# Kernel optimization log

Measured on AMD Instinct MI355X. Metric: run time of the kernel, lower is better.

The kernel has to match this reference:

```python
import jax, jax.numpy as jnp
import numpy as np

DIM = 256
DIM_HEAD = 32
NUM_HEADS = DIM // DIM_HEAD
SCALE = DIM_HEAD ** -0.5


def setup_inputs() -> dict:
    key = jax.random.key(0)
    ks = jax.random.split(key, 5)
    B, L, C = 4, 2048, DIM
    x = jax.random.normal(ks[0], (B, L, C), dtype=jnp.float32)
    # Linear weights stored torch-style: (out_features, in_features)
    w_qkv = jax.random.normal(ks[1], (3 * C, C), dtype=jnp.float32) * (C ** -0.5)
    b_qkv = jax.random.normal(ks[2], (3 * C,), dtype=jnp.float32) * 0.02
    w_proj = jax.random.normal(ks[3], (C, C), dtype=jnp.float32) * (C ** -0.5)
    b_proj = jax.random.normal(ks[4], (C,), dtype=jnp.float32) * 0.02
    return {"x": x, "w_qkv": w_qkv, "b_qkv": b_qkv, "w_proj": w_proj, "b_proj": b_proj}


def reference(x, w_qkv, b_qkv, w_proj, b_proj):
    B, L, C = x.shape
    H, D = NUM_HEADS, DIM_HEAD
    qkv = x @ w_qkv.T + b_qkv                      # (B, L, 3C)
    qkv = qkv.reshape(B, L, H, 3 * D).transpose(0, 2, 1, 3)  # (B, H, L, 3D)
    q, k, v = jnp.split(qkv, 3, axis=-1)           # each (B, H, L, D)
    attn = jnp.einsum('bhld,bhmd->bhlm', q, k) * SCALE
    attn = jax.nn.softmax(attn, axis=-1)
    out = jnp.einsum('bhlm,bhmd->bhld', attn, v)   # (B, H, L, D)
    out = out.transpose(0, 2, 1, 3).reshape(B, L, C)
    return out @ w_proj.T + b_proj
```

## Files before the change

### kernel.cpp

```cpp
#include <hip/hip_runtime.h>
#include <hip/hip_bf16.h>


typedef __bf16 bf16x4 __attribute__((ext_vector_type(4)));
typedef __bf16 bf16x8 __attribute__((ext_vector_type(8)));
typedef float  f32x4  __attribute__((ext_vector_type(4)));
typedef float  f32x16 __attribute__((ext_vector_type(16)));
typedef unsigned u32x4 __attribute__((ext_vector_type(4)));

#define MFMA16(a, b, c) __builtin_amdgcn_mfma_f32_16x16x32_bf16((a), (b), (c), 0, 0, 0)
#define MFMA32(a, b, c) __builtin_amdgcn_mfma_f32_32x32x16_bf16((a), (b), (c), 0, 0, 0)

static constexpr int Bsz = 4, L = 2048, C = 256, H = 8, D = 32;
static constexpr float SCALE = 0.17677669529663687f;
static constexpr float LOG2E = 1.44269504088896f;
static constexpr float QSCALE = SCALE * LOG2E;

__device__ inline float fast_exp2(float x) {
#if __has_builtin(__builtin_amdgcn_exp2f)
    return __builtin_amdgcn_exp2f(x);
#else
    float r; asm("v_exp_f32 %0, %1" : "=v"(r) : "v"(x)); return r;
#endif
}

__device__ inline unsigned cvt_pk_bf16(float lo, float hi) {
    unsigned d;
    asm("v_cvt_pk_bf16_f32 %0, %1, %2" : "=v"(d) : "v"(lo), "v"(hi));
    return d;
}

__global__ __launch_bounds__(256) void qkv_gemm(
    const float* __restrict__ X, const float* __restrict__ W,
    const float* __restrict__ Bq,
    __bf16* __restrict__ Qw, __bf16* __restrict__ Kw, __bf16* __restrict__ Vt)
{
    constexpr int LDK = 136;
    __shared__ __align__(16) __bf16 smem[128 * LDK + 64 * LDK];
    __bf16* Xs = smem;
    __bf16* Wsh = smem + 128 * LDK;

    const int bm = blockIdx.x & 63, bn = blockIdx.x >> 6;
    const int tid = threadIdx.x, wid = tid >> 6, lane = tid & 63;
    const int lr = lane & 15, lh = lane >> 4;
    const int m0b = bm * 128, n0b = bn * 64;
    const int wm0 = (wid >> 1) * 64, wn0 = (wid & 1) * 32;

    const int srow2 = lane >> 5;
    const int scol  = (lane & 31) * 4;

    f32x4 acc[4][2] = {};
    f32x4 xr[16], wr8[8];

#define LOADC(CH) do {                                                        \
    const int k0c = (CH) * 128;                                               \
    _Pragma("unroll")                                                         \
    for (int j = 0; j < 16; ++j) {                                            \
        const int row = j * 8 + wid * 2 + srow2;                              \
        xr[j] = *(const f32x4*)(X + (size_t)(m0b + row) * 256 + k0c + scol);  \
    }                                                                         \
    _Pragma("unroll")                                                         \
    for (int j = 0; j < 8; ++j) {                                             \
        const int row = j * 8 + wid * 2 + srow2;                              \
        wr8[j] = *(const f32x4*)(W + (size_t)(n0b + row) * 256 + k0c + scol); \
    }                                                                         \
} while (0)

#define WRITEC() do {                                                         \
    _Pragma("unroll")                                                         \
    for (int j = 0; j < 16; ++j) {                                            \
        const int row = j * 8 + wid * 2 + srow2;                              \
        bf16x4 cv; cv[0]=(__bf16)xr[j][0]; cv[1]=(__bf16)xr[j][1];            \
                   cv[2]=(__bf16)xr[j][2]; cv[3]=(__bf16)xr[j][3];            \
        *(bf16x4*)(&Xs[row * LDK + scol]) = cv;                               \
    }                                                                         \
    _Pragma("unroll")                                                         \
    for (int j = 0; j < 8; ++j) {                                             \
        const int row = j * 8 + wid * 2 + srow2;                              \
        bf16x4 cv; cv[0]=(__bf16)wr8[j][0]; cv[1]=(__bf16)wr8[j][1];          \
                   cv[2]=(__bf16)wr8[j][2]; cv[3]=(__bf16)wr8[j][3];          \
        *(bf16x4*)(&Wsh[row * LDK + scol]) = cv;                              \
    }                                                                         \
} while (0)

#define COMPUTEC() do {                                                       \
    _Pragma("unroll")                                                         \
    for (int ks = 0; ks < 4; ++ks) {                                          \
        bf16x8 a[4], b[2];                                                    \
        _Pragma("unroll")                                                     \
        for (int mt = 0; mt < 4; ++mt)                                        \
            a[mt] = *(const bf16x8*)(&Xs[(wm0 + mt * 16 + lr) * LDK + ks * 32 + lh * 8]); \
        _Pragma("unroll")                                                     \
        for (int nt = 0; nt < 2; ++nt)                                        \
            b[nt] = *(const bf16x8*)(&Wsh[(wn0 + nt * 16 + lr) * LDK + ks * 32 + lh * 8]); \
        _Pragma("unroll")                                                     \
        for (int mt = 0; mt < 4; ++mt)                                        \
            _Pragma("unroll")                                                 \
            for (int nt = 0; nt < 2; ++nt)                                    \
                acc[mt][nt] = MFMA16(a[mt], b[nt], acc[mt][nt]);              \
    }                                                                         \
} while (0)

    LOADC(0);
    WRITEC();
    LOADC(1);
    __syncthreads();
    COMPUTEC();
    __syncthreads();
    WRITEC();
    __syncthreads();
    COMPUTEC();
    __syncthreads();

#undef LOADC
#undef WRITEC
#undef COMPUTEC

    const int m0 = m0b + wm0;
    const int n0 = n0b + wn0;
    const int bb  = m0 >> 11;
    const int li0 = m0 & 2047;
    const int h = n0 / 96, r = n0 % 96;
    const int which = r >> 5;
    const int bh = bb * H + h;
    __bf16* sw = smem + wid * 2560;

    if (which == 2) {
        #pragma unroll
        for (int nt = 0; nt < 2; ++nt) {
            const float bias = Bq[n0 + nt * 16 + lr];
            #pragma unroll
            for (int mt = 0; mt < 4; ++mt)
                #pragma unroll
                for (int i = 0; i < 4; ++i)
                    sw[(nt * 16 + lr) * 72 + mt * 16 + lh * 4 + i] =
                        (__bf16)(acc[mt][nt][i] + bias);
        }
        #pragma unroll
        for (int j = 0; j < 4; ++j) {
            const int cch = lane + 64 * j;
            const int d = cch >> 3, lc = (cch & 7) * 8;
            const bf16x8 v = *(const bf16x8*)(&sw[d * 72 + lc]);
            *(bf16x8*)(Vt + ((size_t)bh * D + d) * L + li0 + lc) = v;
        }
    } else {
        const float scl = (which == 0) ? QSCALE : 1.0f;
        #pragma unroll
        for (int nt = 0; nt < 2; ++nt) {
            const float bias = Bq[n0 + nt * 16 + lr];
            #pragma unroll
            for (int mt = 0; mt < 4; ++mt)
                #pragma unroll
                for (int i = 0; i < 4; ++i)
                    sw[(mt * 16 + lh * 4 + i) * 40 + nt * 16 + lr] =
                        (__bf16)((acc[mt][nt][i] + bias) * scl);
        }
        __bf16* dst = (which == 0 ? Qw : Kw) + ((size_t)bh * L + li0) * D;
        #pragma unroll
        for (int j = 0; j < 4; ++j) {
            const int cch = lane + 64 * j;
            const bf16x8 v = *(const bf16x8*)(&sw[(cch >> 2) * 40 + (cch & 3) * 8]);
            *(bf16x8*)(dst + (size_t)cch * 8) = v;
        }
    }
}

__global__ __launch_bounds__(256, 4) void attn_fwd(
    const __bf16* __restrict__ Qw, const __bf16* __restrict__ Kw,
    const __bf16* __restrict__ Vt, __bf16* __restrict__ O)
{
    __shared__ __align__(16) __bf16 smem[19456];

    const int bid = blockIdx.x;
    const int bh = ((bid & 7) << 2) | ((bid >> 3) & 3);
    const int qt = bid >> 5;
    const int tid = threadIdx.x, wid = tid >> 6, lane = tid & 63;
    const int lo = lane & 31, hi = lane >> 5;
    const int qgroup = wid & 1, khalf = wid >> 1;
    const int q0 = qt * 64 + qgroup * 32;

    const __bf16* Qb = Qw + (size_t)bh * L * D;
    const __bf16* Kb = Kw + (size_t)bh * L * D;
    const __bf16* Vb = Vt + (size_t)bh * D * L;

    bf16x8 qf[2];
    #pragma unroll
    for (int cl = 0; cl < 2; ++cl)
        qf[cl] = *(const bf16x8*)(Qb + (size_t)(q0 + lo) * D + cl * 16 + hi * 8);

    f32x16 oacc = {};
    float sacc[4] = {0.f, 0.f, 0.f, 0.f};

    const int krow = tid >> 1, kcol = (tid & 1) * 16;
    const int khS = krow >> 6, krl = krow & 63;
    const int vrow = tid >> 2, vcol = (tid & 3) * 16;
    const int vhS = vrow >> 5, vd = vrow & 31;

    bf16x8 kA, kB, vA, vB;
#define LOADR(KV) do {                                                         \
    const __bf16* kp = Kb + (size_t)(khS * 1024 + (KV) + krl) * D + kcol;      \
    kA = *(const bf16x8*)kp;  kB = *(const bf16x8*)(kp + 8);                   \
    const __bf16* vp = Vb + (size_t)vd * L + vhS * 1024 + (KV) + vcol;         \
    vA = *(const bf16x8*)vp;  vB = *(const bf16x8*)(vp + 8);                   \
} while (0)
#define WRITEB(BUF) do {                                                       \
    __bf16* kp = smem + ((BUF) * 2 + khS) * 4864 + krl * 40 + kcol;            \
    *(bf16x8*)kp = kA;  *(bf16x8*)(kp + 8) = kB;                               \
    __bf16* vp = smem + ((BUF) * 2 + vhS) * 4864 + 2560 + vd * 72 + vcol;      \
    *(bf16x8*)vp = vA;  *(bf16x8*)(vp + 8) = vB;                               \
} while (0)

    LOADR(0);
    WRITEB(0);

    for (int t = 0; t < 16; ++t) {
        const int cur = t & 1;
        if (t + 1 < 16) LOADR((t + 1) * 64);
        __syncthreads();

        const __bf16* Kp = smem + (cur * 2 + khalf) * 4864;
        const __bf16* Vp = Kp + 2560;

        #pragma unroll
        for (int sub = 0; sub < 2; ++sub) {
            const int kb = sub * 32;

            f32x16 sst = {};
            const bf16x8 ka0 = *(const bf16x8*)(Kp + (kb + lo) * 40 + hi * 8);
            const bf16x8 ka1 = *(const bf16x8*)(Kp + (kb + lo) * 40 + 16 + hi * 8);
            sst = MFMA32(ka0, qf[0], sst);
            sst = MFMA32(ka1, qf[1], sst);

            float p[16];
            #pragma unroll
            for (int r = 0; r < 16; ++r) p[r] = fast_exp2(sst[r]);
            #pragma unroll
            for (int r = 0; r < 16; ++r) sacc[r & 3] += p[r];

            unsigned pk[8];
            #pragma unroll
            for (int j = 0; j < 8; ++j) pk[j] = cvt_pk_bf16(p[2 * j], p[2 * j + 1]);

            unsigned a0 = pk[0], b0 = pk[2];
            unsigned a1 = pk[1], b1 = pk[3];
            unsigned c0 = pk[4], d0 = pk[6];
            unsigned c1 = pk[5], d1 = pk[7];
            asm("v_permlane32_swap_b32 %0, %1" : "+v"(a0), "+v"(b0));
            asm("v_permlane32_swap_b32 %0, %1" : "+v"(a1), "+v"(b1));
            asm("v_permlane32_swap_b32 %0, %1" : "+v"(c0), "+v"(d0));
            asm("v_permlane32_swap_b32 %0, %1" : "+v"(c1), "+v"(d1));
            const u32x4 f0 = {a0, a1, b0, b1};
            const u32x4 f1 = {c0, c1, d0, d1};
            const bf16x8 pf0 = __builtin_bit_cast(bf16x8, f0);
            const bf16x8 pf1 = __builtin_bit_cast(bf16x8, f1);

            const bf16x8 vb0 = *(const bf16x8*)(Vp + lo * 72 + kb + hi * 8);
            const bf16x8 vb1 = *(const bf16x8*)(Vp + lo * 72 + kb + 16 + hi * 8);
            oacc = MFMA32(pf0, vb0, oacc);
            oacc = MFMA32(pf1, vb1, oacc);
        }

        if (t + 1 < 16) WRITEB(cur ^ 1);
    }
#undef LOADR
#undef WRITEB

    float tot = (sacc[0] + sacc[1]) + (sacc[2] + sacc[3]);
    tot += __shfl_xor(tot, 32);

    __syncthreads();
    float* cs = (float*)smem;
    if (khalf == 1) {
        float* p = cs + (qgroup * 64 + lane) * 20;
        #pragma unroll
        for (int r = 0; r < 16; ++r) p[r] = oacc[r];
        p[16] = tot;
    }
    __syncthreads();
    if (khalf == 0) {
        const float* p = cs + (qgroup * 64 + lane) * 20;
        #pragma unroll
        for (int r = 0; r < 16; ++r) oacc[r] += p[r];
        tot += p[16];
        const float inv = 1.f / tot;

        const int b = bh >> 3, h = bh & 7;
        #pragma unroll
        for (int r = 0; r < 16; ++r) {
            const int qr = (r & 3) + 8 * (r >> 2) + 4 * hi;
            const float rs = __shfl(inv, qr);
            O[((size_t)b * L + q0 + qr) * C + h * D + lo] = (__bf16)(oacc[r] * rs);
        }
    }
}

__global__ __launch_bounds__(256) void proj_gemm(
    const __bf16* __restrict__ A, const float* __restrict__ W,
    const float* __restrict__ Bp, float* __restrict__ Out)
{
    constexpr int LDA = 264;
    __shared__ __align__(16) __bf16 ps[2 * 64 * LDA];
    __bf16* As = ps;
    __bf16* Wsb = ps + 64 * LDA;

    const int bm = blockIdx.x & 127, bn = blockIdx.x >> 7;
    const int tid = threadIdx.x, wid = tid >> 6, lane = tid & 63;
    const int lr = lane & 15, lh = lane >> 4;
    const int m0b = bm * 64, n0b = bn * 64;
    const int wm0 = (wid >> 1) * 32, wn0 = (wid & 1) * 32;

    #pragma unroll
    for (int j = 0; j < 8; ++j) {
        const int c = tid + 256 * j;
        const int row = c >> 5, col = (c & 31) * 8;
        *(bf16x8*)(&As[row * LDA + col]) =
            *(const bf16x8*)(A + (size_t)(m0b + row) * 256 + col);
    }
    #pragma unroll
    for (int j = 0; j < 16; ++j) {
        const int c = tid + 256 * j;
        const int row = c >> 6, col = (c & 63) * 4;
        const f32x4 v = *(const f32x4*)(W + (size_t)(n0b + row) * 256 + col);
        bf16x4 cv; cv[0]=(__bf16)v[0]; cv[1]=(__bf16)v[1]; cv[2]=(__bf16)v[2]; cv[3]=(__bf16)v[3];
        *(bf16x4*)(&Wsb[row * LDA + col]) = cv;
    }
    __syncthreads();

    f32x4 acc[2][2] = {};
    #pragma unroll
    for (int k0 = 0; k0 < 256; k0 += 32) {
        bf16x8 a[2], b[2];
        #pragma unroll
        for (int mt = 0; mt < 2; ++mt)
            a[mt] = *(const bf16x8*)(&As[(wm0 + mt * 16 + lr) * LDA + k0 + lh * 8]);
        #pragma unroll
        for (int nt = 0; nt < 2; ++nt)
            b[nt] = *(const bf16x8*)(&Wsb[(wn0 + nt * 16 + lr) * LDA + k0 + lh * 8]);
        #pragma unroll
        for (int mt = 0; mt < 2; ++mt)
            #pragma unroll
            for (int nt = 0; nt < 2; ++nt)
                acc[mt][nt] = MFMA16(a[mt], b[nt], acc[mt][nt]);
    }

    #pragma unroll
    for (int mt = 0; mt < 2; ++mt) {
        #pragma unroll
        for (int nt = 0; nt < 2; ++nt) {
            const int n = n0b + wn0 + nt * 16 + lr;
            const float bias = Bp[n];
            #pragma unroll
            for (int i = 0; i < 4; ++i) {
                const int m = m0b + wm0 + mt * 16 + lh * 4 + i;
                Out[(size_t)m * 256 + n] = acc[mt][nt][i] + bias;
            }
        }
    }
}

__global__ void fatal_flag(float* Out, int n, float v) {
    int i = blockIdx.x * blockDim.x + threadIdx.x;
    if (i < n) Out[i] = (i == 0) ? v : 0.f;
}

extern "C" void kernel_launch(void* const* d_in, const int* in_sizes, int n_in,
                              void* d_out, int out_size, void* d_ws, size_t ws_size,
                              hipStream_t stream)
{
    float* out = (float*)d_out;

    const float *x = nullptr, *w_qkv = nullptr, *b_qkv = nullptr,
                *w_proj = nullptr, *b_proj = nullptr;
    for (int i = 0; i < n_in; ++i) {
        switch (in_sizes[i]) {
            case 2097152: x      = (const float*)d_in[i]; break;
            case 196608:  w_qkv  = (const float*)d_in[i]; break;
            case 768:     b_qkv  = (const float*)d_in[i]; break;
            case 65536:   w_proj = (const float*)d_in[i]; break;
            case 256:     b_proj = (const float*)d_in[i]; break;
        }
    }
    if (!x || !w_qkv || !b_qkv || !w_proj || !b_proj) {
        fatal_flag<<<dim3((out_size + 255) / 256), dim3(256), 0, stream>>>(out, out_size, 3e9f);
        return;
    }

    const size_t SEG = (size_t)Bsz * H * L * D;
    if (ws_size < 4 * SEG * sizeof(__bf16)) {
        fatal_flag<<<dim3((out_size + 255) / 256), dim3(256), 0, stream>>>(out, out_size, 1e9f);
        return;
    }

    __bf16* ws = (__bf16*)d_ws;
    __bf16* Qw = ws;
    __bf16* Kw = ws + SEG;
    __bf16* Vt = ws + 2 * SEG;
    __bf16* Ob = ws + 3 * SEG;

    qkv_gemm<<<dim3(768), dim3(256), 0, stream>>>(x, w_qkv, b_qkv, Qw, Kw, Vt);
    attn_fwd<<<dim3(1024), dim3(256), 0, stream>>>(Qw, Kw, Vt, Ob);
    proj_gemm<<<dim3(512), dim3(256), 0, stream>>>(Ob, w_proj, b_proj, out);
}
```

Before: 51.67 us.

## Split attention key range across four wave pairs and raise MFMA priority

The attention block grows from 256 to 512 threads, and the key sequence is split into four quarters instead of two. Each wave pair now walks 8 tiles instead of 16, and the partial outputs and row sums of three wave pairs are reduced through shared memory at the end. MFMA instructions are wrapped in s_setprio so matrix work is favoured over other waves. The aim is shorter per-block latency and more waves in flight. The cost is double the LDS per block, which may limit how many blocks fit on a CU, plus a larger final reduction.

```diff
diff --git a/kernel.cpp b/kernel.cpp
--- a/kernel.cpp
+++ b/kernel.cpp
@@ -165,18 +165,18 @@
     }
 }
 
-__global__ __launch_bounds__(256, 4) void attn_fwd(
+__global__ __launch_bounds__(512, 4) void attn_fwd(
     const __bf16* __restrict__ Qw, const __bf16* __restrict__ Kw,
     const __bf16* __restrict__ Vt, __bf16* __restrict__ O)
 {
-    __shared__ __align__(16) __bf16 smem[19456];
+    __shared__ __align__(16) __bf16 smem[38912];
 
     const int bid = blockIdx.x;
     const int bh = ((bid & 7) << 2) | ((bid >> 3) & 3);
     const int qt = bid >> 5;
     const int tid = threadIdx.x, wid = tid >> 6, lane = tid & 63;
     const int lo = lane & 31, hi = lane >> 5;
-    const int qgroup = wid & 1, khalf = wid >> 1;
+    const int qgroup = wid & 1, kq = wid >> 1;
     const int q0 = qt * 64 + qgroup * 32;
 
     const __bf16* Qb = Qw + (size_t)bh * L * D;
@@ -192,33 +192,33 @@
     float sacc[4] = {0.f, 0.f, 0.f, 0.f};
 
     const int krow = tid >> 1, kcol = (tid & 1) * 16;
-    const int khS = krow >> 6, krl = krow & 63;
+    const int kqS = krow >> 6, krl = krow & 63;
     const int vrow = tid >> 2, vcol = (tid & 3) * 16;
-    const int vhS = vrow >> 5, vd = vrow & 31;
+    const int vqS = vrow >> 5, vd = vrow & 31;
 
     bf16x8 kA, kB, vA, vB;
 #define LOADR(KV) do {                                                         \
-    const __bf16* kp = Kb + (size_t)(khS * 1024 + (KV) + krl) * D + kcol;      \
+    const __bf16* kp = Kb + (size_t)(kqS * 512 + (KV) + krl) * D + kcol;       \
     kA = *(const bf16x8*)kp;  kB = *(const bf16x8*)(kp + 8);                   \
-    const __bf16* vp = Vb + (size_t)vd * L + vhS * 1024 + (KV) + vcol;         \
+    const __bf16* vp = Vb + (size_t)vd * L + vqS * 512 + (KV) + vcol;          \
     vA = *(const bf16x8*)vp;  vB = *(const bf16x8*)(vp + 8);                   \
 } while (0)
 #define WRITEB(BUF) do {                                                       \
-    __bf16* kp = smem + ((BUF) * 2 + khS) * 4864 + krl * 40 + kcol;            \
+    __bf16* kp = smem + ((BUF) * 4 + kqS) * 4864 + krl * 40 + kcol;            \
     *(bf16x8*)kp = kA;  *(bf16x8*)(kp + 8) = kB;                               \
-    __bf16* vp = smem + ((BUF) * 2 + vhS) * 4864 + 2560 + vd * 72 + vcol;      \
+    __bf16* vp = smem + ((BUF) * 4 + vqS) * 4864 + 2560 + vd * 72 + vcol;      \
     *(bf16x8*)vp = vA;  *(bf16x8*)(vp + 8) = vB;                               \
 } while (0)
 
     LOADR(0);
     WRITEB(0);
 
-    for (int t = 0; t < 16; ++t) {
+    for (int t = 0; t < 8; ++t) {
         const int cur = t & 1;
-        if (t + 1 < 16) LOADR((t + 1) * 64);
+        if (t + 1 < 8) LOADR((t + 1) * 64);
         __syncthreads();
 
-        const __bf16* Kp = smem + (cur * 2 + khalf) * 4864;
+        const __bf16* Kp = smem + (cur * 4 + kq) * 4864;
         const __bf16* Vp = Kp + 2560;
 
         #pragma unroll
@@ -228,8 +228,10 @@
             f32x16 sst = {};
             const bf16x8 ka0 = *(const bf16x8*)(Kp + (kb + lo) * 40 + hi * 8);
             const bf16x8 ka1 = *(const bf16x8*)(Kp + (kb + lo) * 40 + 16 + hi * 8);
+            __builtin_amdgcn_s_setprio(1);
             sst = MFMA32(ka0, qf[0], sst);
             sst = MFMA32(ka1, qf[1], sst);
+            __builtin_amdgcn_s_setprio(0);
 
             float p[16];
             #pragma unroll
@@ -256,11 +258,13 @@
 
             const bf16x8 vb0 = *(const bf16x8*)(Vp + lo * 72 + kb + hi * 8);
             const bf16x8 vb1 = *(const bf16x8*)(Vp + lo * 72 + kb + 16 + hi * 8);
+            __builtin_amdgcn_s_setprio(1);
             oacc = MFMA32(pf0, vb0, oacc);
             oacc = MFMA32(pf1, vb1, oacc);
-        }
-
-        if (t + 1 < 16) WRITEB(cur ^ 1);
+            __builtin_amdgcn_s_setprio(0);
+        }
+
+        if (t + 1 < 8) WRITEB(cur ^ 1);
     }
 #undef LOADR
 #undef WRITEB
@@ -270,18 +274,21 @@
 
     __syncthreads();
     float* cs = (float*)smem;
-    if (khalf == 1) {
-        float* p = cs + (qgroup * 64 + lane) * 20;
+    if (kq != 0) {
+        float* p = cs + (((kq - 1) * 2 + qgroup) * 64 + lane) * 20;
         #pragma unroll
         for (int r = 0; r < 16; ++r) p[r] = oacc[r];
         p[16] = tot;
     }
     __syncthreads();
-    if (khalf == 0) {
-        const float* p = cs + (qgroup * 64 + lane) * 20;
-        #pragma unroll
-        for (int r = 0; r < 16; ++r) oacc[r] += p[r];
-        tot += p[16];
+    if (kq == 0) {
+        #pragma unroll
+        for (int src = 0; src < 3; ++src) {
+            const float* p = cs + ((src * 2 + qgroup) * 64 + lane) * 20;
+            #pragma unroll
+            for (int r = 0; r < 16; ++r) oacc[r] += p[r];
+            tot += p[16];
+        }
         const float inv = 1.f / tot;
 
         const int b = bh >> 3, h = bh & 7;
@@ -398,6 +405,6 @@
     __bf16* Ob = ws + 3 * SEG;
 
     qkv_gemm<<<dim3(768), dim3(256), 0, stream>>>(x, w_qkv, b_qkv, Qw, Kw, Vt);
-    attn_fwd<<<dim3(1024), dim3(256), 0, stream>>>(Qw, Kw, Vt, Ob);
+    attn_fwd<<<dim3(1024), dim3(512), 0, stream>>>(Qw, Kw, Vt, Ob);
     proj_gemm<<<dim3(512), dim3(256), 0, stream>>>(Ob, w_proj, b_proj, out);
 }
```

Result: slower. 53.23 us (+3.0%).
